# Optimization experiments

Hardware: AMD Instinct MI355X
Metric: run time of the kernel (lower is better)

Reference implementation:

```python
import jax, jax.numpy as jnp
import numpy as np

N = 1048576
NUM_LEVELS = 16; LEVEL_DIM = 2; BASE_RES = 16; TABLE = 1 << 19
BOUND = 1.0; DESIRED = 64
_s = np.exp(np.log(DESIRED / BASE_RES) / (NUM_LEVELS - 1))
RESOLUTIONS = [int(np.floor(BASE_RES * _s ** l)) for l in range(NUM_LEVELS)]
OFFS = np.array([[(i >> 0) & 1, (i >> 1) & 1, (i >> 2) & 1] for i in range(8)], dtype=np.int32)
PRIMES = (1, 2654435761, 805459861)


def _corner_index(corner, R):
    # corner: [N,8,3] int32 in [0,R]. Dense index if grid fits in table, else spatial hash.
    if (R + 1) ** 3 <= TABLE:
        stride = jnp.array([1, R + 1, (R + 1) ** 2], dtype=jnp.int32)
        return jnp.sum(corner * stride, axis=-1)
    c = corner.astype(jnp.uint32)
    h = (c[..., 0] * jnp.uint32(PRIMES[0])) ^ (c[..., 1] * jnp.uint32(PRIMES[1])) ^ (c[..., 2] * jnp.uint32(PRIMES[2]))
    return (h % jnp.uint32(TABLE)).astype(jnp.int32)


def hashgrid_encode(x, embeddings):
    # x: [N,3] in [-BOUND,BOUND]; embeddings: [L, TABLE, C]
    pos = (x + BOUND) / (2.0 * BOUND)  # [0,1]
    offs = jnp.asarray(OFFS)  # [8,3]
    outs = []
    for l, R in enumerate(RESOLUTIONS):  # fixed small loop over levels
        xg = pos * R
        x0 = jnp.clip(jnp.floor(xg).astype(jnp.int32), 0, R - 1)  # [N,3]
        f = xg - x0.astype(xg.dtype)  # trilinear fractions [N,3]
        corners = x0[:, None, :] + offs[None]  # [N,8,3]
        idx = _corner_index(corners, R)  # [N,8]
        feats = embeddings[l][idx]  # [N,8,C] irregular gather
        w = jnp.prod(jnp.where(offs[None] == 1, f[:, None, :], 1.0 - f[:, None, :]), axis=-1)  # [N,8]
        outs.append(jnp.sum(feats * w[..., None], axis=1))  # [N,C]
    return jnp.concatenate(outs, axis=-1)  # [N, L*C] = [N,32]


def sh_encode(d):
    # degree-4 real spherical harmonics (16 coeffs), torch-ngp convention
    x, y, z = d[..., 0], d[..., 1], d[..., 2]
    xx, yy, zz = x * x, y * y, z * z
    xy, yz, xz = x * y, y * z, x * z
    return jnp.stack([
        0.28209479177387814 * jnp.ones_like(x),
        -0.48860251190291987 * y,
        0.48860251190291987 * z,
        -0.48860251190291987 * x,
        1.0925484305920792 * xy,
        -1.0925484305920792 * yz,
        0.94617469575755997 * zz - 0.31539156525252005,
        -1.0925484305920792 * xz,
        0.54627421529603959 * (xx - yy),
        0.59004358992664352 * y * (yy - 3.0 * xx),
        2.8906114426405538 * xy * z,
        0.45704579946446572 * y * (1.0 - 5.0 * zz),
        0.3731763325901154 * z * (5.0 * zz - 3.0),
        0.45704579946446572 * x * (1.0 - 5.0 * zz),
        1.4453057213202769 * z * (xx - yy),
        0.59004358992664352 * x * (3.0 * yy - xx),
    ], axis=-1)  # [N,16]


def setup_inputs() -> dict:
    key = jax.random.key(0)
    ks = jax.random.split(key, 8)
    x = jax.random.uniform(ks[0], (N, 3), jnp.float32) * 2.0 - 1.0  # in [-bound, bound]
    d_raw = jax.random.normal(ks[1], (N, 3), jnp.float32)
    d = d_raw / (jnp.linalg.norm(d_raw, axis=-1, keepdims=True) + 1e-8)  # unit view dirs
    embeddings = jax.random.normal(ks[2], (NUM_LEVELS, TABLE, LEVEL_DIM), jnp.float32) * 1e-2
    def w(k, i, o):
        return jax.random.normal(k, (i, o), jnp.float32) / np.sqrt(i).astype(np.float32)
    ws0 = w(ks[3], 32, 64)
    ws1 = w(ks[4], 64, 16)
    wc0 = w(ks[5], 31, 64)
    wc1 = w(ks[6], 64, 64)
    wc2 = w(ks[7], 64, 1)
    return {"x": x, "d": d, "embeddings": embeddings,
            "ws0": ws0, "ws1": ws1, "wc0": wc0, "wc1": wc1, "wc2": wc2}


def reference(x, d, embeddings, ws0, ws1, wc0, wc1, wc2):
    # sigma branch: hashgrid encode -> 2-layer bias-free MLP
    h = hashgrid_encode(x, embeddings)          # [N,32]
    h = jax.nn.relu(h @ ws0) @ ws1              # [N,16]
    sigma = jnp.abs(h[:, :1])                   # [N,1]
    geo_feat = h[:, 1:]                         # [N,15]
    # color branch: SH encode dir, concat geo feature, 3-layer bias-free MLP
    hd = jnp.concatenate([sh_encode(d), geo_feat], axis=-1)  # [N,31]
    c = jax.nn.relu(hd @ wc0)
    c = jax.nn.relu(c @ wc1)
    color = jnp.abs(c @ wc2)                    # [N,1]
    return sigma, color
```

## Files before the change

kernel.cpp:

```cpp
#include <hip/hip_runtime.h>
#include <cmath>

#define NPTS 1048576
#define TABLE_SZ 524288
#define NBUCK 32768

typedef _Float16 half8 __attribute__((ext_vector_type(8)));
typedef _Float16 half4 __attribute__((ext_vector_type(4)));
typedef _Float16 h2 __attribute__((ext_vector_type(2)));
typedef float floatx4 __attribute__((ext_vector_type(4)));
typedef unsigned int uint2a4 __attribute__((ext_vector_type(2), aligned(4)));

#define MFMA16x16x32 __builtin_amdgcn_mfma_f32_16x16x32_f16

__device__ __forceinline__ h2 as_h2(unsigned int u) {
    union { unsigned int u; h2 h; } c; c.u = u; return c.h;
}

__global__ void prepack_weights(const float* __restrict__ ws0,
                                const float* __restrict__ ws1,
                                const float* __restrict__ wc0,
                                const float* __restrict__ wc1,
                                const float* __restrict__ wc2,
                                half8* __restrict__ wfrag)
{
    const int f = blockIdx.x, l = threadIdx.x;
    const float* W; int Kreal, Mreal, mt, kt;
    if (f < 4)       { W = ws0; Kreal = 32; Mreal = 64; mt = f;          kt = 0;        }
    else if (f < 6)  { W = ws1; Kreal = 64; Mreal = 16; mt = 0;          kt = f - 4;    }
    else if (f < 10) { W = wc0; Kreal = 31; Mreal = 64; mt = f - 6;      kt = 0;        }
    else if (f < 18) { W = wc1; Kreal = 64; Mreal = 64; mt = (f-10)>>1;  kt = (f-10)&1; }
    else             { W = wc2; Kreal = 64; Mreal = 1;  mt = 0;          kt = f - 18;   }

    const int m  = 16*mt + (l & 15);
    const int k0 = 32*kt + (l >> 4)*8;
    half8 hv;
    #pragma unroll
    for (int e = 0; e < 8; ++e) {
        const int k = k0 + e;
        const float v = (m < Mreal && k < Kreal) ? W[k*Mreal + m] : 0.0f;
        hv[e] = (_Float16)v;
    }
    wfrag[f*64 + l] = hv;
}

__global__ __launch_bounds__(256) void convert_tables(
    const float* __restrict__ emb, unsigned int* __restrict__ tabu,
    unsigned int* __restrict__ hist, int zero_hist,
    int4 ra, int4 rb, int4 rc, int4 rd,
    int4 oa, int4 ob, int4 oc, int4 od)
{
    const int l = blockIdx.y;
    if (l == 16) {
        if (zero_hist) {
            const int e = blockIdx.x * 256 + threadIdx.x;
            if (e < NBUCK) hist[e] = 0u;
        }
        return;
    }
    const int q = l >> 2, j = l & 3;
    const int4 rv = (q == 0) ? ra : (q == 1) ? rb : (q == 2) ? rc : rd;
    const int4 ov = (q == 0) ? oa : (q == 1) ? ob : (q == 2) ? oc : od;
    const int R   = (j == 0) ? rv.x : (j == 1) ? rv.y : (j == 2) ? rv.z : rv.w;
    const int off = (j == 0) ? ov.x : (j == 1) ? ov.y : (j == 2) ? ov.z : ov.w;
    const int n = (R+1)*(R+1)*(R+1);
    const int e = blockIdx.x * 256 + threadIdx.x;
    if (e >= n) return;
    const float2 v = *(const float2*)(emb + (size_t)l * (TABLE_SZ*2) + 2*(size_t)e);
    union { unsigned int u; _Float16 h[2]; } c;
    c.h[0] = (_Float16)v.x; c.h[1] = (_Float16)v.y;
    tabu[off + e] = c.u;
}

__device__ __forceinline__ int bucket_of(float px, float py, float pz) {
    int bx = (int)(px * 32.0f); bx = bx < 0 ? 0 : (bx > 31 ? 31 : bx);
    int by = (int)(py * 32.0f); by = by < 0 ? 0 : (by > 31 ? 31 : by);
    int bz = (int)(pz * 32.0f); bz = bz < 0 ? 0 : (bz > 31 ? 31 : bz);
    return bx | (by << 5) | (bz << 10);
}

__global__ __launch_bounds__(256) void hist_kernel(
    const float* __restrict__ xin, unsigned int* __restrict__ hist,
    unsigned int* __restrict__ rnk)
{
    const int i = blockIdx.x * 256 + threadIdx.x;
    const float px = (xin[3*i+0] + 1.0f) * 0.5f;
    const float py = (xin[3*i+1] + 1.0f) * 0.5f;
    const float pz = (xin[3*i+2] + 1.0f) * 0.5f;
    rnk[i] = atomicAdd(&hist[bucket_of(px, py, pz)], 1u);
}

__global__ __launch_bounds__(1024) void scan_kernel(
    const unsigned int* __restrict__ hist, unsigned int* __restrict__ off)
{
    __shared__ unsigned int ssum[1024];
    const int t = threadIdx.x;
    unsigned int v[32];
    unsigned int s = 0;
    #pragma unroll
    for (int j = 0; j < 32; ++j) {
        const unsigned int h = hist[t*32 + j];
        v[j] = s; s += h;
    }
    ssum[t] = s;
    __syncthreads();
    for (int d = 1; d < 1024; d <<= 1) {
        const unsigned int add = (t >= d) ? ssum[t-d] : 0u;
        __syncthreads();
        ssum[t] += add;
        __syncthreads();
    }
    const unsigned int base = (t == 0) ? 0u : ssum[t-1];
    #pragma unroll
    for (int j = 0; j < 32; ++j) off[t*32 + j] = base + v[j];
}

__global__ __launch_bounds__(256) void scatter_kernel(
    const float* __restrict__ xin, const unsigned int* __restrict__ boff,
    const unsigned int* __restrict__ rnk, float4* __restrict__ xs4)
{
    const int i = blockIdx.x * 256 + threadIdx.x;
    const float px = (xin[3*i+0] + 1.0f) * 0.5f;
    const float py = (xin[3*i+1] + 1.0f) * 0.5f;
    const float pz = (xin[3*i+2] + 1.0f) * 0.5f;
    const int b = bucket_of(px, py, pz);
    const unsigned int pos = boff[b] + rnk[i];
    xs4[pos] = make_float4(px, py, pz, __uint_as_float((unsigned int)i));
}

__global__ __launch_bounds__(256, 4) void ngp_gather_sorted(
    const float4* __restrict__ xs4, const unsigned int* __restrict__ tabu,
    _Float16* __restrict__ feats,
    int4 ra, int4 rb, int4 rc, int4 rd,
    int4 oa, int4 ob, int4 oc, int4 od)
{
    const int p = blockIdx.x * 256 + threadIdx.x;
    const int q = blockIdx.y;

    const float4 xv = xs4[p];
    const float px = xv.x, py = xv.y, pz = xv.z;

    const int4 rv = (q == 0) ? ra : (q == 1) ? rb : (q == 2) ? rc : rd;
    const int4 ov = (q == 0) ? oa : (q == 1) ? ob : (q == 2) ? oc : od;

    uint2a4 P[16];
    float fx[4], fy[4], fz[4];

    #pragma unroll
    for (int j = 0; j < 4; ++j) {
        const int R   = (j == 0) ? rv.x : (j == 1) ? rv.y : (j == 2) ? rv.z : rv.w;
        const int off = (j == 0) ? ov.x : (j == 1) ? ov.y : (j == 2) ? ov.z : ov.w;
        const float Rf = (float)R;
        const float gx = px*Rf, gy = py*Rf, gz = pz*Rf;
        int x0 = (int)floorf(gx); x0 = x0 < 0 ? 0 : (x0 > R-1 ? R-1 : x0);
        int y0 = (int)floorf(gy); y0 = y0 < 0 ? 0 : (y0 > R-1 ? R-1 : y0);
        int z0 = (int)floorf(gz); z0 = z0 < 0 ? 0 : (z0 > R-1 ? R-1 : z0);
        fx[j] = gx - (float)x0; fy[j] = gy - (float)y0; fz[j] = gz - (float)z0;
        const int s1 = R + 1, s2 = s1 * s1;
        const unsigned int* tab = tabu + off;
        const int b = x0 + y0*s1 + z0*s2;
        P[4*j+0] = *(const uint2a4*)(tab + b);
        P[4*j+1] = *(const uint2a4*)(tab + b + s1);
        P[4*j+2] = *(const uint2a4*)(tab + b + s2);
        P[4*j+3] = *(const uint2a4*)(tab + b + s1 + s2);
    }

    union { half8 v; h2 h[4]; } hv;
    #pragma unroll
    for (int j = 0; j < 4; ++j) {
        const _Float16 fxh = (_Float16)fx[j];
        const _Float16 fyh = (_Float16)fy[j];
        const _Float16 fzh = (_Float16)fz[j];
        const h2 fx2 = {fxh, fxh}, fy2 = {fyh, fyh}, fz2 = {fzh, fzh};
        const h2 c000 = as_h2(P[4*j+0].x), c100 = as_h2(P[4*j+0].y);
        const h2 c010 = as_h2(P[4*j+1].x), c110 = as_h2(P[4*j+1].y);
        const h2 c001 = as_h2(P[4*j+2].x), c101 = as_h2(P[4*j+2].y);
        const h2 c011 = as_h2(P[4*j+3].x), c111 = as_h2(P[4*j+3].y);
        const h2 a00 = c000 + fx2 * (c100 - c000);
        const h2 a10 = c010 + fx2 * (c110 - c010);
        const h2 a01 = c001 + fx2 * (c101 - c001);
        const h2 a11 = c011 + fx2 * (c111 - c011);
        const h2 b0  = a00 + fy2 * (a10 - a00);
        const h2 b1  = a01 + fy2 * (a11 - a01);
        hv.h[j] = b0 + fz2 * (b1 - b0);
    }
    *(half8*)&feats[((size_t)q * NPTS + p) * 8] = hv.v;
}

__global__ __launch_bounds__(256, 4) void ngp_gather_lin(
    const float* __restrict__ xin, const unsigned int* __restrict__ tabu,
    _Float16* __restrict__ feats,
    int4 ra, int4 rb, int4 rc, int4 rd,
    int4 oa, int4 ob, int4 oc, int4 od)
{
    const int tid = blockIdx.x * 256 + threadIdx.x;
    const int p = tid >> 2;
    const int q = tid & 3;

    const float px = (xin[3*p+0] + 1.0f) * 0.5f;
    const float py = (xin[3*p+1] + 1.0f) * 0.5f;
    const float pz = (xin[3*p+2] + 1.0f) * 0.5f;

    const int4 rv = (q == 0) ? ra : (q == 1) ? rb : (q == 2) ? rc : rd;
    const int4 ov = (q == 0) ? oa : (q == 1) ? ob : (q == 2) ? oc : od;

    uint2a4 P[16];
    float fx[4], fy[4], fz[4];
    #pragma unroll
    for (int j = 0; j < 4; ++j) {
        const int R   = (j == 0) ? rv.x : (j == 1) ? rv.y : (j == 2) ? rv.z : rv.w;
        const int off = (j == 0) ? ov.x : (j == 1) ? ov.y : (j == 2) ? ov.z : ov.w;
        const float Rf = (float)R;
        const float gx = px*Rf, gy = py*Rf, gz = pz*Rf;
        int x0 = (int)floorf(gx); x0 = x0 < 0 ? 0 : (x0 > R-1 ? R-1 : x0);
        int y0 = (int)floorf(gy); y0 = y0 < 0 ? 0 : (y0 > R-1 ? R-1 : y0);
        int z0 = (int)floorf(gz); z0 = z0 < 0 ? 0 : (z0 > R-1 ? R-1 : z0);
        fx[j] = gx - (float)x0; fy[j] = gy - (float)y0; fz[j] = gz - (float)z0;
        const int s1 = R + 1, s2 = s1 * s1;
        const unsigned int* tab = tabu + off;
        const int b = x0 + y0*s1 + z0*s2;
        P[4*j+0] = *(const uint2a4*)(tab + b);
        P[4*j+1] = *(const uint2a4*)(tab + b + s1);
        P[4*j+2] = *(const uint2a4*)(tab + b + s2);
        P[4*j+3] = *(const uint2a4*)(tab + b + s1 + s2);
    }
    union { half8 v; h2 h[4]; } hv;
    #pragma unroll
    for (int j = 0; j < 4; ++j) {
        const _Float16 fxh = (_Float16)fx[j];
        const _Float16 fyh = (_Float16)fy[j];
        const _Float16 fzh = (_Float16)fz[j];
        const h2 fx2 = {fxh, fxh}, fy2 = {fyh, fyh}, fz2 = {fzh, fzh};
        const h2 c000 = as_h2(P[4*j+0].x), c100 = as_h2(P[4*j+0].y);
        const h2 c010 = as_h2(P[4*j+1].x), c110 = as_h2(P[4*j+1].y);
        const h2 c001 = as_h2(P[4*j+2].x), c101 = as_h2(P[4*j+2].y);
        const h2 c011 = as_h2(P[4*j+3].x), c111 = as_h2(P[4*j+3].y);
        const h2 a00 = c000 + fx2 * (c100 - c000);
        const h2 a10 = c010 + fx2 * (c110 - c010);
        const h2 a01 = c001 + fx2 * (c101 - c001);
        const h2 a11 = c011 + fx2 * (c111 - c011);
        const h2 b0  = a00 + fy2 * (a10 - a00);
        const h2 b1  = a01 + fy2 * (a11 - a01);
        hv.h[j] = b0 + fz2 * (b1 - b0);
    }
    *(half8*)&feats[(size_t)p*32 + q*8] = hv.v;
}

template<int SORTED>
__global__ __launch_bounds__(256) void ngp_mlp(
    const float* __restrict__ din, const _Float16* __restrict__ feats,
    const float4* __restrict__ xs4,
    const half8* __restrict__ wfrag, float* __restrict__ out)
{
    __shared__ __align__(16) _Float16 smM[4][32][72];
    __shared__ __align__(16) _Float16 smG[4][32][24];

    const int tid  = threadIdx.x;
    const int w    = tid >> 6, lane = tid & 63;
    const int gbase = (blockIdx.x * 4 + w) * 32;

    const int n = lane & 15, g = lane >> 4;
    const floatx4 zz = {0.f, 0.f, 0.f, 0.f};

    unsigned int orig0, orig1;
    if (SORTED) {
        orig0 = __float_as_uint(xs4[gbase + n].w);
        orig1 = __float_as_uint(xs4[gbase + 16 + n].w);
    } else {
        orig0 = gbase + n;
        orig1 = gbase + 16 + n;
    }

    auto storeQ = [&](int pt, int mt, floatx4 a) {
        half4 hv;
        hv[0] = (_Float16)fmaxf(a[0], 0.f); hv[1] = (_Float16)fmaxf(a[1], 0.f);
        hv[2] = (_Float16)fmaxf(a[2], 0.f); hv[3] = (_Float16)fmaxf(a[3], 0.f);
        *(half4*)&smM[w][pt][16*mt + 4*g] = hv;
    };

    {
        const half8 A0 = wfrag[0*64+lane], A1 = wfrag[1*64+lane];
        const half8 A2 = wfrag[2*64+lane], A3 = wfrag[3*64+lane];
        #pragma unroll
        for (int nt = 0; nt < 2; ++nt) {
            const int pt = nt*16 + n;
            half8 B;
            if (SORTED)
                B = *(const half8*)&feats[((size_t)g * NPTS + (gbase + pt)) * 8];
            else
                B = *(const half8*)&feats[(size_t)(gbase + pt)*32 + 8*g];
            floatx4 a0 = MFMA16x16x32(A0, B, zz, 0,0,0);
            floatx4 a1 = MFMA16x16x32(A1, B, zz, 0,0,0);
            floatx4 a2 = MFMA16x16x32(A2, B, zz, 0,0,0);
            floatx4 a3 = MFMA16x16x32(A3, B, zz, 0,0,0);
            storeQ(pt, 0, a0); storeQ(pt, 1, a1); storeQ(pt, 2, a2); storeQ(pt, 3, a3);
        }
    }
    asm volatile("" ::: "memory");

    {
        const half8 A0 = wfrag[4*64+lane], A1 = wfrag[5*64+lane];
        #pragma unroll
        for (int nt = 0; nt < 2; ++nt) {
            const int pt = nt*16 + n;
            const half8 B0 = *(const half8*)&smM[w][pt][ 0 + 8*g];
            const half8 B1 = *(const half8*)&smM[w][pt][32 + 8*g];
            floatx4 acc = MFMA16x16x32(A0, B0, zz, 0,0,0);
            acc = MFMA16x16x32(A1, B1, acc, 0,0,0);
            if (g == 0) {
                out[nt ? orig1 : orig0] = fabsf(acc[0]);
                smG[w][pt][0]  = (_Float16)acc[1];
                smG[w][pt][1]  = (_Float16)acc[2];
                smG[w][pt][2]  = (_Float16)acc[3];
                smG[w][pt][15] = (_Float16)0.f;
            } else {
                smG[w][pt][4*g-1] = (_Float16)acc[0];
                smG[w][pt][4*g+0] = (_Float16)acc[1];
                smG[w][pt][4*g+1] = (_Float16)acc[2];
                smG[w][pt][4*g+2] = (_Float16)acc[3];
            }
        }
    }
    asm volatile("" ::: "memory");

    {
        const half8 A0 = wfrag[6*64+lane], A1 = wfrag[7*64+lane];
        const half8 A2 = wfrag[8*64+lane], A3 = wfrag[9*64+lane];
        #pragma unroll
        for (int nt = 0; nt < 2; ++nt) {
            const int pt = nt*16 + n;
            half8 B;
            if (g < 2) {
                const unsigned int gpt = nt ? orig1 : orig0;
                const float x = din[3*gpt+0], y = din[3*gpt+1], z = din[3*gpt+2];
                const float xx = x*x, yy = y*y, zzq = z*z;
                const float xy = x*y, yz = y*z, xz = x*z;
                float s[8];
                if (g == 0) {
                    s[0] = 0.28209479177387814f;
                    s[1] = -0.48860251190291987f * y;
                    s[2] =  0.48860251190291987f * z;
                    s[3] = -0.48860251190291987f * x;
                    s[4] =  1.0925484305920792f * xy;
                    s[5] = -1.0925484305920792f * yz;
                    s[6] =  0.94617469575756f * zzq - 0.31539156525252005f;
                    s[7] = -1.0925484305920792f * xz;
                } else {
                    s[0] =  0.5462742152960396f * (xx - yy);
                    s[1] =  0.5900435899266435f * y * (yy - 3.0f*xx);
                    s[2] =  2.890611442640554f * xy * z;
                    s[3] =  0.4570457994644657f * y * (1.0f - 5.0f*zzq);
                    s[4] =  0.3731763325901154f * z * (5.0f*zzq - 3.0f);
                    s[5] =  0.4570457994644657f * x * (1.0f - 5.0f*zzq);
                    s[6] =  1.445305721320277f * z * (xx - yy);
                    s[7] =  0.5900435899266435f * x * (3.0f*yy - xx);
                }
                #pragma unroll
                for (int e = 0; e < 8; ++e) B[e] = (_Float16)s[e];
            } else {
                B = *(const half8*)&smG[w][pt][8*(g-2)];
            }
            floatx4 a0 = MFMA16x16x32(A0, B, zz, 0,0,0);
            floatx4 a1 = MFMA16x16x32(A1, B, zz, 0,0,0);
            floatx4 a2 = MFMA16x16x32(A2, B, zz, 0,0,0);
            floatx4 a3 = MFMA16x16x32(A3, B, zz, 0,0,0);
            storeQ(pt, 0, a0); storeQ(pt, 1, a1); storeQ(pt, 2, a2); storeQ(pt, 3, a3);
        }
    }
    asm volatile("" ::: "memory");

    {
        const half8 A0 = wfrag[10*64+lane], A1 = wfrag[11*64+lane];
        const half8 A2 = wfrag[12*64+lane], A3 = wfrag[13*64+lane];
        const half8 A4 = wfrag[14*64+lane], A5 = wfrag[15*64+lane];
        const half8 A6 = wfrag[16*64+lane], A7 = wfrag[17*64+lane];
        #pragma unroll
        for (int nt = 0; nt < 2; ++nt) {
            const int pt = nt*16 + n;
            const half8 B0 = *(const half8*)&smM[w][pt][ 0 + 8*g];
            const half8 B1 = *(const half8*)&smM[w][pt][32 + 8*g];
            floatx4 a0 = MFMA16x16x32(A0, B0, zz, 0,0,0); a0 = MFMA16x16x32(A1, B1, a0, 0,0,0);
            floatx4 a1 = MFMA16x16x32(A2, B0, zz, 0,0,0); a1 = MFMA16x16x32(A3, B1, a1, 0,0,0);
            floatx4 a2 = MFMA16x16x32(A4, B0, zz, 0,0,0); a2 = MFMA16x16x32(A5, B1, a2, 0,0,0);
            floatx4 a3 = MFMA16x16x32(A6, B0, zz, 0,0,0); a3 = MFMA16x16x32(A7, B1, a3, 0,0,0);
            storeQ(pt, 0, a0); storeQ(pt, 1, a1); storeQ(pt, 2, a2); storeQ(pt, 3, a3);
        }
    }
    asm volatile("" ::: "memory");

    {
        const half8 A0 = wfrag[18*64+lane], A1 = wfrag[19*64+lane];
        #pragma unroll
        for (int nt = 0; nt < 2; ++nt) {
            const int pt = nt*16 + n;
            const half8 B0 = *(const half8*)&smM[w][pt][ 0 + 8*g];
            const half8 B1 = *(const half8*)&smM[w][pt][32 + 8*g];
            floatx4 acc = MFMA16x16x32(A0, B0, zz, 0,0,0);
            acc = MFMA16x16x32(A1, B1, acc, 0,0,0);
            if (g == 0) out[NPTS + (nt ? orig1 : orig0)] = fabsf(acc[0]);
        }
    }
}

extern "C" void kernel_launch(void* const* d_in, const int* in_sizes, int n_in,
                              void* d_out, int out_size, void* d_ws, size_t ws_size,
                              hipStream_t stream)
{
    const float* x   = (const float*)d_in[0];
    const float* d   = (const float*)d_in[1];
    const float* emb = (const float*)d_in[2];
    const float* ws0 = (const float*)d_in[3];
    const float* ws1 = (const float*)d_in[4];
    const float* wc0 = (const float*)d_in[5];
    const float* wc1 = (const float*)d_in[6];
    const float* wc2 = (const float*)d_in[7];
    float* out = (float*)d_out;

    const size_t OFF_WFRAG = 0;
    const size_t OFF_TABU  = 32768;
    const size_t OFF_FEATS = OFF_TABU + 8388608;
    const size_t OFF_HIST  = OFF_FEATS + 67108864;
    const size_t OFF_OFF   = OFF_HIST + NBUCK*4;
    const size_t OFF_XS4   = OFF_OFF + NBUCK*4;
    const size_t OFF_RNK   = OFF_XS4 + (size_t)NPTS*16;
    const size_t NEED_SORT = OFF_RNK + (size_t)NPTS*4;
    const size_t NEED_LIN  = OFF_HIST;

    half8* wfrag        = (half8*)((char*)d_ws + OFF_WFRAG);
    unsigned int* tabu  = (unsigned int*)((char*)d_ws + OFF_TABU);
    _Float16* feats     = (_Float16*)((char*)d_ws + OFF_FEATS);
    unsigned int* hist  = (unsigned int*)((char*)d_ws + OFF_HIST);
    unsigned int* boff  = (unsigned int*)((char*)d_ws + OFF_OFF);
    float4* xs4         = (float4*)((char*)d_ws + OFF_XS4);
    unsigned int* rnk   = (unsigned int*)((char*)d_ws + OFF_RNK);

    int r[16], off[16];
    const double s = std::exp(std::log(4.0) / 15.0);
    int acc = 0;
    for (int l = 0; l < 16; ++l) {
        r[l] = (int)std::floor(16.0 * std::pow(s, (double)l));
        off[l] = acc;
        acc += (r[l]+1)*(r[l]+1)*(r[l]+1);
    }
    const int4 ra = {r[0],  r[1],  r[2],  r[3]};
    const int4 rb = {r[4],  r[5],  r[6],  r[7]};
    const int4 rc = {r[8],  r[9],  r[10], r[11]};
    const int4 rd = {r[12], r[13], r[14], r[15]};
    const int4 oa = {off[0],  off[1],  off[2],  off[3]};
    const int4 ob = {off[4],  off[5],  off[6],  off[7]};
    const int4 oc = {off[8],  off[9],  off[10], off[11]};
    const int4 od = {off[12], off[13], off[14], off[15]};

    prepack_weights<<<20, 64, 0, stream>>>(ws0, ws1, wc0, wc1, wc2, wfrag);

    const int nmax = (r[15]+1)*(r[15]+1)*(r[15]+1);
    dim3 cgrid((nmax + 255) / 256, 17);

    if (ws_size >= NEED_SORT) {
        convert_tables<<<cgrid, 256, 0, stream>>>(emb, tabu, hist, 1, ra, rb, rc, rd, oa, ob, oc, od);
        hist_kernel<<<NPTS/256, 256, 0, stream>>>(x, hist, rnk);
        scan_kernel<<<1, 1024, 0, stream>>>(hist, boff);
        scatter_kernel<<<NPTS/256, 256, 0, stream>>>(x, boff, rnk, xs4);
        dim3 ggrid(NPTS/256, 4);
        ngp_gather_sorted<<<ggrid, 256, 0, stream>>>(xs4, tabu, feats, ra, rb, rc, rd, oa, ob, oc, od);
        ngp_mlp<1><<<NPTS/128, 256, 0, stream>>>(d, feats, xs4, wfrag, out);
    } else if (ws_size >= NEED_LIN) {
        convert_tables<<<cgrid, 256, 0, stream>>>(emb, tabu, hist, 0, ra, rb, rc, rd, oa, ob, oc, od);
        ngp_gather_lin<<<NPTS*4/256, 256, 0, stream>>>(x, tabu, feats, ra, rb, rc, rd, oa, ob, oc, od);
        ngp_mlp<0><<<NPTS/128, 256, 0, stream>>>(d, feats, (const float4*)nullptr, wfrag, out);
    }
}
```

Baseline: 192.3 us.

## Pass geo features between MLP layers via lane shuffles instead of shared memory

```diff
diff --git a/kernel.cpp b/kernel.cpp
--- a/kernel.cpp
+++ b/kernel.cpp
@@ -8,6 +8,7 @@
 typedef _Float16 half8 __attribute__((ext_vector_type(8)));
 typedef _Float16 half4 __attribute__((ext_vector_type(4)));
 typedef _Float16 h2 __attribute__((ext_vector_type(2)));
+typedef __fp16 fp16x2 __attribute__((ext_vector_type(2)));
 typedef float floatx4 __attribute__((ext_vector_type(4)));
 typedef unsigned int uint2a4 __attribute__((ext_vector_type(2), aligned(4)));
 
@@ -15,6 +16,11 @@
 
 __device__ __forceinline__ h2 as_h2(unsigned int u) {
     union { unsigned int u; h2 h; } c; c.u = u; return c.h;
+}
+__device__ __forceinline__ unsigned int pk_u32(float a, float b) {
+    union { fp16x2 h; unsigned int u; } c;
+    c.h = __builtin_amdgcn_cvt_pkrtz(a, b);
+    return c.u;
 }
 
 __global__ void prepack_weights(const float* __restrict__ ws0,
@@ -25,19 +31,35 @@
                                 half8* __restrict__ wfrag)
 {
     const int f = blockIdx.x, l = threadIdx.x;
+    const int lane_m = l & 15, k0 = (l >> 4) * 8;
+    half8 hv;
+
+    if (f >= 6 && f < 10) {
+        const int m = 16*(f-6) + lane_m;
+        #pragma unroll
+        for (int e = 0; e < 8; ++e) {
+            const int k = k0 + e;
+            float v;
+            if (k < 16)       v = wc0[k*64 + m];
+            else if (k == 16) v = 0.0f;
+            else              v = wc0[(k-1)*64 + m];
+            hv[e] = (_Float16)v;
+        }
+        wfrag[f*64 + l] = hv;
+        return;
+    }
+
     const float* W; int Kreal, Mreal, mt, kt;
     if (f < 4)       { W = ws0; Kreal = 32; Mreal = 64; mt = f;          kt = 0;        }
     else if (f < 6)  { W = ws1; Kreal = 64; Mreal = 16; mt = 0;          kt = f - 4;    }
-    else if (f < 10) { W = wc0; Kreal = 31; Mreal = 64; mt = f - 6;      kt = 0;        }
     else if (f < 18) { W = wc1; Kreal = 64; Mreal = 64; mt = (f-10)>>1;  kt = (f-10)&1; }
     else             { W = wc2; Kreal = 64; Mreal = 1;  mt = 0;          kt = f - 18;   }
 
-    const int m  = 16*mt + (l & 15);
-    const int k0 = 32*kt + (l >> 4)*8;
-    half8 hv;
+    const int m  = 16*mt + lane_m;
+    const int kk0 = 32*kt + k0;
     #pragma unroll
     for (int e = 0; e < 8; ++e) {
-        const int k = k0 + e;
+        const int k = kk0 + e;
         const float v = (m < Mreal && k < Kreal) ? W[k*Mreal + m] : 0.0f;
         hv[e] = (_Float16)v;
     }
@@ -67,9 +89,7 @@
     const int e = blockIdx.x * 256 + threadIdx.x;
     if (e >= n) return;
     const float2 v = *(const float2*)(emb + (size_t)l * (TABLE_SZ*2) + 2*(size_t)e);
-    union { unsigned int u; _Float16 h[2]; } c;
-    c.h[0] = (_Float16)v.x; c.h[1] = (_Float16)v.y;
-    tabu[off + e] = c.u;
+    tabu[off + e] = pk_u32(v.x, v.y);
 }
 
 __device__ __forceinline__ int bucket_of(float px, float py, float pz) {
@@ -252,8 +272,7 @@
     const float4* __restrict__ xs4,
     const half8* __restrict__ wfrag, float* __restrict__ out)
 {
-    __shared__ __align__(16) _Float16 smM[4][32][72];
-    __shared__ __align__(16) _Float16 smG[4][32][24];
+    __shared__ __align__(16) _Float16 smM[4][32][88];
 
     const int tid  = threadIdx.x;
     const int w    = tid >> 6, lane = tid & 63;
@@ -271,24 +290,31 @@
         orig1 = gbase + 16 + n;
     }
 
+    const float dX0 = din[3*orig0+0], dY0 = din[3*orig0+1], dZ0 = din[3*orig0+2];
+    const float dX1 = din[3*orig1+0], dY1 = din[3*orig1+1], dZ1 = din[3*orig1+2];
+
     auto storeQ = [&](int pt, int mt, floatx4 a) {
-        half4 hv;
-        hv[0] = (_Float16)fmaxf(a[0], 0.f); hv[1] = (_Float16)fmaxf(a[1], 0.f);
-        hv[2] = (_Float16)fmaxf(a[2], 0.f); hv[3] = (_Float16)fmaxf(a[3], 0.f);
-        *(half4*)&smM[w][pt][16*mt + 4*g] = hv;
+        union { unsigned int u[2]; half4 v; } c;
+        c.u[0] = pk_u32(fmaxf(a[0], 0.f), fmaxf(a[1], 0.f));
+        c.u[1] = pk_u32(fmaxf(a[2], 0.f), fmaxf(a[3], 0.f));
+        *(half4*)&smM[w][pt][16*mt + 4*g] = c.v;
     };
 
     {
         const half8 A0 = wfrag[0*64+lane], A1 = wfrag[1*64+lane];
         const half8 A2 = wfrag[2*64+lane], A3 = wfrag[3*64+lane];
+        half8 B0, B1;
+        if (SORTED) {
+            B0 = *(const half8*)&feats[((size_t)g * NPTS + (gbase + n)) * 8];
+            B1 = *(const half8*)&feats[((size_t)g * NPTS + (gbase + 16 + n)) * 8];
+        } else {
+            B0 = *(const half8*)&feats[(size_t)(gbase + n)*32 + 8*g];
+            B1 = *(const half8*)&feats[(size_t)(gbase + 16 + n)*32 + 8*g];
+        }
         #pragma unroll
         for (int nt = 0; nt < 2; ++nt) {
             const int pt = nt*16 + n;
-            half8 B;
-            if (SORTED)
-                B = *(const half8*)&feats[((size_t)g * NPTS + (gbase + pt)) * 8];
-            else
-                B = *(const half8*)&feats[(size_t)(gbase + pt)*32 + 8*g];
+            const half8 B = nt ? B1 : B0;
             floatx4 a0 = MFMA16x16x32(A0, B, zz, 0,0,0);
             floatx4 a1 = MFMA16x16x32(A1, B, zz, 0,0,0);
             floatx4 a2 = MFMA16x16x32(A2, B, zz, 0,0,0);
@@ -298,27 +324,33 @@
     }
     asm volatile("" ::: "memory");
 
+    unsigned int s1w0_0, s1w0_1, s1w1_0, s1w1_1;
     {
         const half8 A0 = wfrag[4*64+lane], A1 = wfrag[5*64+lane];
-        #pragma unroll
-        for (int nt = 0; nt < 2; ++nt) {
-            const int pt = nt*16 + n;
+        float sig0, sig1;
+        {
+            const int pt = n;
             const half8 B0 = *(const half8*)&smM[w][pt][ 0 + 8*g];
             const half8 B1 = *(const half8*)&smM[w][pt][32 + 8*g];
             floatx4 acc = MFMA16x16x32(A0, B0, zz, 0,0,0);
             acc = MFMA16x16x32(A1, B1, acc, 0,0,0);
-            if (g == 0) {
-                out[nt ? orig1 : orig0] = fabsf(acc[0]);
-                smG[w][pt][0]  = (_Float16)acc[1];
-                smG[w][pt][1]  = (_Float16)acc[2];
-                smG[w][pt][2]  = (_Float16)acc[3];
-                smG[w][pt][15] = (_Float16)0.f;
-            } else {
-                smG[w][pt][4*g-1] = (_Float16)acc[0];
-                smG[w][pt][4*g+0] = (_Float16)acc[1];
-                smG[w][pt][4*g+1] = (_Float16)acc[2];
-                smG[w][pt][4*g+2] = (_Float16)acc[3];
-            }
+            s1w0_0 = pk_u32(acc[0], acc[1]);
+            s1w0_1 = pk_u32(acc[2], acc[3]);
+            sig0 = acc[0];
+        }
+        {
+            const int pt = 16 + n;
+            const half8 B0 = *(const half8*)&smM[w][pt][ 0 + 8*g];
+            const half8 B1 = *(const half8*)&smM[w][pt][32 + 8*g];
+            floatx4 acc = MFMA16x16x32(A0, B0, zz, 0,0,0);
+            acc = MFMA16x16x32(A1, B1, acc, 0,0,0);
+            s1w1_0 = pk_u32(acc[0], acc[1]);
+            s1w1_1 = pk_u32(acc[2], acc[3]);
+            sig1 = acc[0];
+        }
+        if (g == 0) {
+            out[orig0] = fabsf(sig0);
+            out[orig1] = fabsf(sig1);
         }
     }
     asm volatile("" ::: "memory");
@@ -326,13 +358,21 @@
     {
         const half8 A0 = wfrag[6*64+lane], A1 = wfrag[7*64+lane];
         const half8 A2 = wfrag[8*64+lane], A3 = wfrag[9*64+lane];
+        const int srcA = ((g & 1) << 5) + n;
         #pragma unroll
         for (int nt = 0; nt < 2; ++nt) {
             const int pt = nt*16 + n;
-            half8 B;
+            const unsigned int v0 = nt ? s1w1_0 : s1w0_0;
+            const unsigned int v1 = nt ? s1w1_1 : s1w0_1;
+            const unsigned int w0 = __shfl(v0, srcA);
+            const unsigned int w1 = __shfl(v1, srcA);
+            const unsigned int w2 = __shfl(v0, srcA + 16);
+            const unsigned int w3 = __shfl(v1, srcA + 16);
+            union { half8 v; unsigned int u[4]; } B;
             if (g < 2) {
-                const unsigned int gpt = nt ? orig1 : orig0;
-                const float x = din[3*gpt+0], y = din[3*gpt+1], z = din[3*gpt+2];
+                const float x = nt ? dX1 : dX0;
+                const float y = nt ? dY1 : dY0;
+                const float z = nt ? dZ1 : dZ0;
                 const float xx = x*x, yy = y*y, zzq = z*z;
                 const float xy = x*y, yz = y*z, xz = x*z;
                 float s[8];
@@ -355,15 +395,15 @@
                     s[6] =  1.445305721320277f * z * (xx - yy);
                     s[7] =  0.5900435899266435f * x * (3.0f*yy - xx);
                 }
-                #pragma unroll
-                for (int e = 0; e < 8; ++e) B[e] = (_Float16)s[e];
+                B.u[0] = pk_u32(s[0], s[1]); B.u[1] = pk_u32(s[2], s[3]);
+                B.u[2] = pk_u32(s[4], s[5]); B.u[3] = pk_u32(s[6], s[7]);
             } else {
-                B = *(const half8*)&smG[w][pt][8*(g-2)];
+                B.u[0] = w0; B.u[1] = w1; B.u[2] = w2; B.u[3] = w3;
             }
-            floatx4 a0 = MFMA16x16x32(A0, B, zz, 0,0,0);
-            floatx4 a1 = MFMA16x16x32(A1, B, zz, 0,0,0);
-            floatx4 a2 = MFMA16x16x32(A2, B, zz, 0,0,0);
-            floatx4 a3 = MFMA16x16x32(A3, B, zz, 0,0,0);
+            floatx4 a0 = MFMA16x16x32(A0, B.v, zz, 0,0,0);
+            floatx4 a1 = MFMA16x16x32(A1, B.v, zz, 0,0,0);
+            floatx4 a2 = MFMA16x16x32(A2, B.v, zz, 0,0,0);
+            floatx4 a3 = MFMA16x16x32(A3, B.v, zz, 0,0,0);
             storeQ(pt, 0, a0); storeQ(pt, 1, a1); storeQ(pt, 2, a2); storeQ(pt, 3, a3);
         }
     }
```

New measurement: 194.1 us. About the same (+0.9%).
